# Kernel optimization log

Hardware: AMD Instinct MI355X
Metric: run time of the kernel (lower is better)

## Reference

```python
import jax, jax.numpy as jnp
import numpy as np

N = 100000      # nodes
E = 1600000     # edges (avg degree 16)
IN_DIM = 128
HID = 128
OUT = 10
EPS = 1e-5      # BatchNorm eps


def _lin(key, fan_in, fan_out):
    return jax.random.normal(key, (fan_in, fan_out), jnp.float32) * (1.0 / np.sqrt(fan_in))


def setup_inputs() -> dict:
    key = jax.random.key(0)
    ks = jax.random.split(key, 8)
    x = jax.random.normal(ks[0], (N, IN_DIM), jnp.float32)
    edge_index = jax.random.randint(ks[1], (2, E), 0, N, dtype=jnp.int64)
    return {
        "x": x,
        "edge_index": edge_index,
        "W0": _lin(ks[2], IN_DIM, HID), "b0": jnp.zeros((HID,), jnp.float32),
        "g0": jnp.ones((HID,), jnp.float32), "be0": jnp.zeros((HID,), jnp.float32),
        "W1": _lin(ks[3], HID, HID), "b1": jnp.zeros((HID,), jnp.float32),
        "g1": jnp.ones((HID,), jnp.float32), "be1": jnp.zeros((HID,), jnp.float32),
        "W2": _lin(ks[4], HID, OUT), "b2": jnp.zeros((OUT,), jnp.float32),
    }


def gcn_conv(x, W, b, src, dst, n):
    # PyG GCNConv: add self-loops, symmetric normalization D^-1/2 A D^-1/2.
    # deg includes the self-loop (+1).
    e = src.shape[0]
    deg = jax.ops.segment_sum(jnp.ones((e,), x.dtype), dst, num_segments=n) + 1.0
    dinv = jax.lax.rsqrt(deg)                     # deg >= 1 always
    norm = dinv[src] * dinv[dst]                  # [E]
    h = x @ W                                     # [N, out]
    msgs = h[src] * norm[:, None]                 # gather + scale, [E, out]
    agg = jax.ops.segment_sum(msgs, dst, num_segments=n)
    agg = agg + h * (dinv * dinv)[:, None]        # self-loop contribution
    return agg + b


def batch_norm(x, gamma, beta):
    mu = jnp.mean(x, axis=0)
    var = jnp.mean(jnp.square(x - mu), axis=0)    # biased var, as torch BN training
    return gamma * (x - mu) * jax.lax.rsqrt(var + EPS) + beta


def reference(x, edge_index, W0, b0, g0, be0, W1, b1, g1, be1, W2, b2):
    src, dst = edge_index[0], edge_index[1]
    h = jax.nn.relu(batch_norm(gcn_conv(x, W0, b0, src, dst, N), g0, be0))
    h = jax.nn.relu(batch_norm(gcn_conv(h, W1, b1, src, dst, N), g1, be1))
    return gcn_conv(h, W2, b2, src, dst, N)
```

## Files before the change

kernel.cpp:

```cpp
#include <hip/hip_runtime.h>
#include <hip/hip_bf16.h>

static constexpr int NN  = 100000;
static constexpr int NE  = 1600000;
static constexpr int DIM = 128;
static constexpr int OC  = 10;
static constexpr int BK  = 64;
static constexpr float BN_EPS = 1e-5f;
static constexpr float INVN   = 1.0f / (float)NN;

typedef unsigned short ushortT;
typedef unsigned int uintT;
typedef __attribute__((ext_vector_type(8))) short short8;
typedef __attribute__((ext_vector_type(4))) float floatx4;

__device__ __forceinline__ ushortT f2bf(float f) {
    union { float f; unsigned int i; } c;
    c.f = f;
    unsigned int r = c.i + 0x7FFFu + ((c.i >> 16) & 1u);
    return (ushortT)(r >> 16);
}

__device__ __forceinline__ uintT pack2(float lo, float hi) {
    return (uintT)f2bf(lo) | ((uintT)f2bf(hi) << 16);
}

__device__ __forceinline__ float4 f4fma(const float4 w, const float s, const float4 acc) {
    float4 r;
    r.x = fmaf(w.x, s, acc.x);
    r.y = fmaf(w.y, s, acc.y);
    r.z = fmaf(w.z, s, acc.z);
    r.w = fmaf(w.w, s, acc.w);
    return r;
}

__device__ __forceinline__ void acc8(const uint4 u, float* a) {
    a[0] += __uint_as_float(u.x << 16);
    a[1] += __uint_as_float(u.x & 0xFFFF0000u);
    a[2] += __uint_as_float(u.y << 16);
    a[3] += __uint_as_float(u.y & 0xFFFF0000u);
    a[4] += __uint_as_float(u.z << 16);
    a[5] += __uint_as_float(u.z & 0xFFFF0000u);
    a[6] += __uint_as_float(u.w << 16);
    a[7] += __uint_as_float(u.w & 0xFFFF0000u);
}

__device__ __forceinline__ void fma8(const uint4 u, float s, float* a) {
    a[0] = fmaf(__uint_as_float(u.x << 16),          s, a[0]);
    a[1] = fmaf(__uint_as_float(u.x & 0xFFFF0000u),  s, a[1]);
    a[2] = fmaf(__uint_as_float(u.y << 16),          s, a[2]);
    a[3] = fmaf(__uint_as_float(u.y & 0xFFFF0000u),  s, a[3]);
    a[4] = fmaf(__uint_as_float(u.z << 16),          s, a[4]);
    a[5] = fmaf(__uint_as_float(u.z & 0xFFFF0000u),  s, a[5]);
    a[6] = fmaf(__uint_as_float(u.w << 16),          s, a[6]);
    a[7] = fmaf(__uint_as_float(u.w & 0xFFFF0000u),  s, a[7]);
}

__device__ __forceinline__ void unp8(const uint4 u, float* a) {
    a[0] = __uint_as_float(u.x << 16);
    a[1] = __uint_as_float(u.x & 0xFFFF0000u);
    a[2] = __uint_as_float(u.y << 16);
    a[3] = __uint_as_float(u.y & 0xFFFF0000u);
    a[4] = __uint_as_float(u.z << 16);
    a[5] = __uint_as_float(u.z & 0xFFFF0000u);
    a[6] = __uint_as_float(u.w << 16);
    a[7] = __uint_as_float(u.w & 0xFFFF0000u);
}

__global__ void k_wt(const float* __restrict__ W0, const float* __restrict__ W1,
                     ushortT* __restrict__ WT0, ushortT* __restrict__ WT1,
                     float* __restrict__ stats) {
    int i = blockIdx.x * 256 + threadIdx.x;
    if (i < 512) stats[i] = 0.f;
    int half = i >> 14, r = i & 16383;
    int n = r >> 7, k = r & 127;
    if (half == 0) WT0[r] = f2bf(W0[k * 128 + n]);
    else           WT1[r] = f2bf(W1[k * 128 + n]);
}

__global__ __launch_bounds__(256, 8)
void k_fused(const int* __restrict__ src, const int* __restrict__ dst,
             int* __restrict__ cnt, int* __restrict__ bucket,
             const float* __restrict__ x, const ushortT* __restrict__ WT,
             ushortT* __restrict__ outb)
{
    const int idx = blockIdx.x;
    const int m = idx / 3, r3 = idx - 3 * m;
    if (r3 < 2) {
        int e = (2 * m + r3) * 256 + threadIdx.x;
        if (e < NE) {
            int t = dst[e];
            int slot = atomicAdd(&cnt[t], 1);
            if (slot < BK)
                __hip_atomic_store(&bucket[(size_t)t * BK + slot], src[e],
                                   __ATOMIC_RELAXED, __HIP_MEMORY_SCOPE_AGENT);
        }
        return;
    }
    __shared__ ushortT XS[32 * 136];
    const int tid  = threadIdx.x;
    const int row0 = m * 32;

    #pragma unroll
    for (int i = 0; i < 4; ++i) {
        int id2 = tid + 256 * i;
        int rr = id2 >> 5, c4 = id2 & 31;
        int grow = row0 + rr;
        float4 v = {0.f, 0.f, 0.f, 0.f};
        if (grow < NN) v = ((const float4*)(x + (size_t)grow * DIM))[c4];
        ushort4 o;
        o.x = f2bf(v.x); o.y = f2bf(v.y); o.z = f2bf(v.z); o.w = f2bf(v.w);
        *(ushort4*)(XS + rr * 136 + c4 * 4) = o;
    }
    __syncthreads();

    const int w    = tid >> 6;
    const int lane = tid & 63;
    const int q    = lane >> 4;
    const int mr   = lane & 15;
    const int rw   = (w >> 1) * 16;
    const int ch   = (w & 1) * 64;

    floatx4 acc[4];
    #pragma unroll
    for (int t = 0; t < 4; ++t) { acc[t][0] = 0.f; acc[t][1] = 0.f; acc[t][2] = 0.f; acc[t][3] = 0.f; }

    #pragma unroll
    for (int c = 0; c < 4; ++c) {
        short8 a = *(const short8*)(XS + (rw + mr) * 136 + c * 32 + q * 8);
        #pragma unroll
        for (int t = 0; t < 4; ++t) {
            short8 b = *(const short8*)(WT + (size_t)(ch + t * 16 + mr) * 128 + c * 32 + q * 8);
            acc[t] = __builtin_amdgcn_mfma_f32_16x16x32_bf16(a, b, acc[t], 0, 0, 0);
        }
    }

    #pragma unroll
    for (int rr = 0; rr < 4; ++rr) {
        int grow = row0 + rw + q * 4 + rr;
        if (grow < NN) {
            #pragma unroll
            for (int t = 0; t < 4; ++t)
                outb[(size_t)grow * DIM + ch + t * 16 + mr] = f2bf(acc[t][rr]);
        }
    }
}

__global__ void k_dinv(const int* __restrict__ cnt, float* __restrict__ dinv, int n) {
    int i = blockIdx.x * 256 + threadIdx.x;
    if (i < n) dinv[i] = rsqrtf((float)cnt[i] + 1.0f);
}

template <bool EDGE_SCALE>
__global__ __launch_bounds__(256)
void k_agg_wide(const ushortT* __restrict__ hb, const int* __restrict__ cnt,
                const int* __restrict__ bucket, const float* __restrict__ dinv,
                const float* __restrict__ bias, ushortT* __restrict__ outBb,
                float* __restrict__ stats)
{
    const int lane = threadIdx.x & 63;
    const int w    = threadIdx.x >> 6;
    const int sg   = lane >> 4;
    const int f    = lane & 15;
    const int wid  = blockIdx.x * 4 + w;
    const int nW   = gridDim.x * 4;
    const uint4* h4 = (const uint4*)hb;

    float bl[8];
    #pragma unroll
    for (int i = 0; i < 8; ++i) bl[i] = bias[f * 8 + i];

    float ssum[8], ssq[8];
    #pragma unroll
    for (int i = 0; i < 8; ++i) { ssum[i] = 0.f; ssq[i] = 0.f; }

    for (int n = wid; n < NN; n += nW) {
        int d = cnt[n];
        if (d > BK) d = BK;
        const int* bp = bucket + (size_t)n * BK;
        float a[8];
        #pragma unroll
        for (int i = 0; i < 8; ++i) a[i] = 0.f;

        int j = 0;
        for (; j + 16 <= d; j += 16) {
            int4 pv = *(const int4*)(bp + j + 4 * sg);
            uint4 u0 = h4[(size_t)pv.x * 16 + f];
            uint4 u1 = h4[(size_t)pv.y * 16 + f];
            uint4 u2 = h4[(size_t)pv.z * 16 + f];
            uint4 u3 = h4[(size_t)pv.w * 16 + f];
            if (EDGE_SCALE) {
                float d0 = dinv[pv.x], d1 = dinv[pv.y];
                float d2 = dinv[pv.z], d3 = dinv[pv.w];
                fma8(u0, d0, a);
                fma8(u1, d1, a);
                fma8(u2, d2, a);
                fma8(u3, d3, a);
            } else {
                acc8(u0, a);
                acc8(u1, a);
                acc8(u2, a);
                acc8(u3, a);
            }
        }
        for (; j + 8 <= d; j += 8) {
            int s0 = bp[j + sg];
            int s1 = bp[j + 4 + sg];
            uint4 u0 = h4[(size_t)s0 * 16 + f];
            uint4 u1 = h4[(size_t)s1 * 16 + f];
            if (EDGE_SCALE) {
                float d0 = dinv[s0], d1 = dinv[s1];
                fma8(u0, d0, a);
                fma8(u1, d1, a);
            } else {
                acc8(u0, a);
                acc8(u1, a);
            }
        }
        for (; j < d; j += 4) {
            int e = j + sg;
            if (e < d) {
                int s0 = bp[e];
                uint4 u = h4[(size_t)s0 * 16 + f];
                if (EDGE_SCALE) fma8(u, dinv[s0], a);
                else            acc8(u, a);
            }
        }
        #pragma unroll
        for (int i = 0; i < 8; ++i) {
            a[i] += __shfl_xor(a[i], 16);
            a[i] += __shfl_xor(a[i], 32);
        }
        if (lane < 16) {
            uint4 us = h4[(size_t)n * 16 + f];
            float di = dinv[n];
            if (EDGE_SCALE) fma8(us, di, a);
            else            acc8(us, a);
            float v[8];
            #pragma unroll
            for (int i = 0; i < 8; ++i) v[i] = fmaf(di, a[i], bl[i]);
            uint4 o;
            o.x = pack2(v[0], v[1]);
            o.y = pack2(v[2], v[3]);
            o.z = pack2(v[4], v[5]);
            o.w = pack2(v[6], v[7]);
            ((uint4*)(outBb + (size_t)n * DIM))[f] = o;
            #pragma unroll
            for (int i = 0; i < 8; ++i) {
                ssum[i] += v[i];
                ssq[i]  = fmaf(v[i], v[i], ssq[i]);
            }
        }
    }

    __shared__ float ls[4 * 128], lq[4 * 128];
    if (lane < 16) {
        #pragma unroll
        for (int i = 0; i < 8; ++i) {
            ls[w * 128 + f * 8 + i] = ssum[i];
            lq[w * 128 + f * 8 + i] = ssq[i];
        }
    }
    __syncthreads();
    int t = threadIdx.x;
    if (t < 128) {
        float a = ls[t] + ls[128 + t] + ls[256 + t] + ls[384 + t];
        float b = lq[t] + lq[128 + t] + lq[256 + t] + lq[384 + t];
        unsafeAtomicAdd(&stats[t], a);
        unsafeAtomicAdd(&stats[128 + t], b);
    }
}

__global__ __launch_bounds__(256)
void k_mm128_l1(const ushortT* __restrict__ inb, const ushortT* __restrict__ WT,
                const float* __restrict__ stats, const float* __restrict__ g,
                const float* __restrict__ be, const float* __restrict__ dinv,
                ushortT* __restrict__ outb)
{
    __shared__ ushortT XS[64 * 136];
    __shared__ float CA[128], CD[128];
    const int tid  = threadIdx.x;
    const int row0 = blockIdx.x * 64;

    if (tid < 128) {
        float mu  = stats[tid] * INVN;
        float var = stats[128 + tid] * INVN - mu * mu;
        float a = g[tid] * rsqrtf(var + BN_EPS);
        CA[tid] = a;
        CD[tid] = be[tid] - mu * a;
    }
    __syncthreads();

    #pragma unroll
    for (int i = 0; i < 4; ++i) {
        int idx = tid + 256 * i;
        int r = idx >> 4, c8 = idx & 15;
        int grow = row0 + r;
        uint4 u = {0, 0, 0, 0};
        if (grow < NN) u = ((const uint4*)(inb + (size_t)grow * DIM))[c8];
        float v[8];
        unp8(u, v);
        #pragma unroll
        for (int k = 0; k < 8; ++k)
            v[k] = fmaxf(0.f, fmaf(v[k], CA[c8 * 8 + k], CD[c8 * 8 + k]));
        uint4 o;
        o.x = pack2(v[0], v[1]);
        o.y = pack2(v[2], v[3]);
        o.z = pack2(v[4], v[5]);
        o.w = pack2(v[6], v[7]);
        *(uint4*)(XS + r * 136 + c8 * 8) = o;
    }
    __syncthreads();

    const int w    = tid >> 6;
    const int lane = tid & 63;
    const int q    = lane >> 4;
    const int mr   = lane & 15;
    const int rw   = w * 16;

    floatx4 acc[8];
    #pragma unroll
    for (int t = 0; t < 8; ++t) { acc[t][0] = 0.f; acc[t][1] = 0.f; acc[t][2] = 0.f; acc[t][3] = 0.f; }

    #pragma unroll
    for (int c = 0; c < 4; ++c) {
        short8 a = *(const short8*)(XS + (rw + mr) * 136 + c * 32 + q * 8);
        #pragma unroll
        for (int t = 0; t < 8; ++t) {
            short8 b = *(const short8*)(WT + (size_t)(t * 16 + mr) * 128 + c * 32 + q * 8);
            acc[t] = __builtin_amdgcn_mfma_f32_16x16x32_bf16(a, b, acc[t], 0, 0, 0);
        }
    }

    #pragma unroll
    for (int r = 0; r < 4; ++r) {
        int grow = row0 + rw + q * 4 + r;
        if (grow < NN) {
            float di = dinv[grow];
            #pragma unroll
            for (int t = 0; t < 8; ++t) {
                outb[(size_t)grow * DIM + t * 16 + mr] = f2bf(acc[t][r] * di);
            }
        }
    }
}

__global__ __launch_bounds__(128)
void k_mm_l2(const ushortT* __restrict__ inb, const float* __restrict__ W2,
             const float* __restrict__ stats, const float* __restrict__ g,
             const float* __restrict__ be, const float* __restrict__ dinv,
             ushortT* __restrict__ Cb)
{
    __shared__ float WL[128 * 16];
    __shared__ float XS[32 * 128];
    __shared__ float CA[128], CD[128];
    const int tid  = threadIdx.x;
    const int row0 = blockIdx.x * 32;

    {
        float mu  = stats[tid] * INVN;
        float var = stats[128 + tid] * INVN - mu * mu;
        float a = g[tid] * rsqrtf(var + BN_EPS);
        CA[tid] = a;
        CD[tid] = be[tid] - mu * a;
    }
    for (int idx = tid; idx < 128 * 16; idx += 128) {
        int k = idx >> 4, c = idx & 15;
        WL[idx] = (c < OC) ? W2[k * OC + c] : 0.0f;
    }
    __syncthreads();

    #pragma unroll
    for (int i = 0; i < 4; ++i) {
        int idx = tid + 128 * i;
        int r = idx >> 4, c8 = idx & 15;
        uint4 u = ((const uint4*)(inb + (size_t)(row0 + r) * DIM))[c8];
        float v[8];
        unp8(u, v);
        float* xp = XS + r * 128 + c8 * 8;
        #pragma unroll
        for (int k = 0; k < 8; ++k)
            xp[k] = fmaxf(0.f, fmaf(v[k], CA[c8 * 8 + k], CD[c8 * 8 + k]));
    }
    __syncthreads();

    const int cg = tid & 3;
    const int rg = tid >> 2;
    float4 acc = {0, 0, 0, 0};
    const float4* XS4 = (const float4*)XS;
    const float4* WL4 = (const float4*)WL;
    for (int k = 0; k < 128; k += 4) {
        float4 w0 = WL4[(k + 0) * 4 + cg];
        float4 w1 = WL4[(k + 1) * 4 + cg];
        float4 w2 = WL4[(k + 2) * 4 + cg];
        float4 w3 = WL4[(k + 3) * 4 + cg];
        float4 x = XS4[rg * 32 + (k >> 2)];
        acc = f4fma(w0, x.x, f4fma(w1, x.y, f4fma(w2, x.z, f4fma(w3, x.w, acc))));
    }
    float di = dinv[row0 + rg];
    uint2 o;
    o.x = pack2(acc.x * di, acc.y * di);
    o.y = pack2(acc.z * di, acc.w * di);
    ((uint2*)(Cb + ((size_t)row0 + rg) * 16))[cg] = o;
}

__global__ __launch_bounds__(256)
void k_agg10(const ushortT* __restrict__ Cb, const int* __restrict__ cnt,
             const int* __restrict__ bucket, const float* __restrict__ dinv,
             const float* __restrict__ b2, float* __restrict__ out)
{
    const int lane = threadIdx.x & 63;
    const int sg   = lane >> 3;
    const int f    = lane & 7;
    const int wid  = (blockIdx.x * 256 + threadIdx.x) >> 6;
    const int nW   = gridDim.x * 4;
    const uintT* Cu = (const uintT*)Cb;

    for (int n = wid; n < NN; n += nW) {
        int d = cnt[n];
        if (d > BK) d = BK;
        const int* bp = bucket + (size_t)n * BK;
        float a0 = 0.f, a1 = 0.f;
        for (int j = sg; j < d; j += 8) {
            uintT u = Cu[(size_t)bp[j] * 8 + f];
            a0 += __uint_as_float(u << 16);
            a1 += __uint_as_float(u & 0xFFFF0000u);
        }
        a0 += __shfl_xor(a0, 8);  a1 += __shfl_xor(a1, 8);
        a0 += __shfl_xor(a0, 16); a1 += __shfl_xor(a1, 16);
        a0 += __shfl_xor(a0, 32); a1 += __shfl_xor(a1, 32);
        if (lane < 8) {
            uintT us = Cu[(size_t)n * 8 + f];
            a0 += __uint_as_float(us << 16);
            a1 += __uint_as_float(us & 0xFFFF0000u);
            float di = dinv[n];
            if (2 * f < OC) {
                float2 o;
                o.x = fmaf(di, a0, b2[2 * f]);
                o.y = fmaf(di, a1, b2[2 * f + 1]);
                *(float2*)(out + (size_t)n * OC + 2 * f) = o;
            }
        }
    }
}

extern "C" void kernel_launch(void* const* d_in, const int* in_sizes, int n_in,
                              void* d_out, int out_size, void* d_ws, size_t ws_size,
                              hipStream_t stream) {
    const float* x    = (const float*)d_in[0];
    const int*   ei   = (const int*)d_in[1];
    const int*   srcv = ei;
    const int*   dstv = ei + NE;
    const float* W0  = (const float*)d_in[2];
    const float* b0  = (const float*)d_in[3];
    const float* g0  = (const float*)d_in[4];
    const float* be0 = (const float*)d_in[5];
    const float* W1  = (const float*)d_in[6];
    const float* b1  = (const float*)d_in[7];
    const float* g1  = (const float*)d_in[8];
    const float* be1 = (const float*)d_in[9];
    const float* W2  = (const float*)d_in[10];
    const float* b2  = (const float*)d_in[11];
    float* out = (float*)d_out;

    float* base   = (float*)d_ws;
    int*   cnt    = (int*)base;
    float* dinv   = base + NN;
    float* stats  = base + 2 * NN;
    ushortT* WT0  = (ushortT*)(base + 2 * NN + 512);
    ushortT* WT1  = (ushortT*)(base + 2 * NN + 8704);
    int*   bucket = (int*)(base + 2 * NN + 16896);
    ushortT* A_bf = (ushortT*)(base + 2 * NN + 16896 + (size_t)NN * BK);
    ushortT* B_bf = A_bf + (size_t)NN * DIM;
    ushortT* Cb   = A_bf;

    (void)hipMemsetAsync(cnt, 0, NN * sizeof(int), stream);

    k_wt<<<128, 256, 0, stream>>>(W0, W1, WT0, WT1, stats);

    k_fused<<<9375, 256, 0, stream>>>(srcv, dstv, cnt, bucket, x, WT0, A_bf);
    k_dinv<<<(NN + 255) / 256, 256, 0, stream>>>(cnt, dinv, NN);

    k_agg_wide<true><<<2048, 256, 0, stream>>>(A_bf, cnt, bucket, dinv, b0, B_bf, stats);

    k_mm128_l1<<<(NN + 63) / 64, 256, 0, stream>>>(B_bf, WT1, stats, g0, be0, dinv, A_bf);
    k_agg_wide<false><<<2048, 256, 0, stream>>>(A_bf, cnt, bucket, dinv, b1, B_bf, stats + 256);

    k_mm_l2<<<NN / 32, 128, 0, stream>>>(B_bf, W2, stats + 256, g1, be1, dinv, Cb);
    k_agg10<<<1024, 256, 0, stream>>>(Cb, cnt, bucket, dinv, b2, out);
}
```

Measured before the change: 535.4 us.

## Replace global-atomic edge bucketing with two-pass binned counting sort

Global atomics on per-node counters and scattered bucket stores are replaced by a two-pass scheme. In the first pass, blocks sort 4096-edge chunks into 256-node bins in shared memory and write padded runs to per-bin global regions. In the second pass, one block per bin builds the node buckets with shared-memory atomics and computes degree and dinv, which removes the memset and the separate dinv kernel. The trade-offs are extra passes over edge data and a fixed per-bin capacity that could overflow and silently drop edges on skewed graphs.

```diff
diff --git a/kernel.cpp b/kernel.cpp
--- a/kernel.cpp
+++ b/kernel.cpp
@@ -8,6 +8,10 @@
 static constexpr int BK  = 64;
 static constexpr float BN_EPS = 1e-5f;
 static constexpr float INVN   = 1.0f / (float)NN;
+
+static constexpr int BINS = 391;
+static constexpr int CAP  = 8176;
+static constexpr int P1B  = (NE + 4095) / 4096;
 
 typedef unsigned short ushortT;
 typedef unsigned int uintT;
@@ -71,34 +75,111 @@
                      ushortT* __restrict__ WT0, ushortT* __restrict__ WT1,
                      float* __restrict__ stats) {
     int i = blockIdx.x * 256 + threadIdx.x;
-    if (i < 512) stats[i] = 0.f;
+    if (i < 1024) stats[i] = 0.f;
     int half = i >> 14, r = i & 16383;
     int n = r >> 7, k = r & 127;
     if (half == 0) WT0[r] = f2bf(W0[k * 128 + n]);
     else           WT1[r] = f2bf(W1[k * 128 + n]);
 }
 
-__global__ __launch_bounds__(256, 8)
-void k_fused(const int* __restrict__ src, const int* __restrict__ dst,
-             int* __restrict__ cnt, int* __restrict__ bucket,
-             const float* __restrict__ x, const ushortT* __restrict__ WT,
-             ushortT* __restrict__ outb)
+struct P1S {
+    uint2 stage[4096];
+    int lcnt[BINS];
+    int lbase[512];
+    int lcur[BINS];
+    int goff[BINS];
+};
+union SMu {
+    P1S p1;
+    ushortT xs[32 * 136];
+};
+
+__global__ __launch_bounds__(256)
+void k_p1(const int* __restrict__ src, const int* __restrict__ dst,
+          uint2* __restrict__ gbin, int* __restrict__ gcur,
+          const float* __restrict__ x, const ushortT* __restrict__ WT,
+          ushortT* __restrict__ outb)
 {
+    __shared__ SMu sm;
     const int idx = blockIdx.x;
-    const int m = idx / 3, r3 = idx - 3 * m;
-    if (r3 < 2) {
-        int e = (2 * m + r3) * 256 + threadIdx.x;
-        if (e < NE) {
-            int t = dst[e];
-            int slot = atomicAdd(&cnt[t], 1);
-            if (slot < BK)
-                __hip_atomic_store(&bucket[(size_t)t * BK + slot], src[e],
-                                   __ATOMIC_RELAXED, __HIP_MEMORY_SCOPE_AGENT);
+    const int tid = threadIdx.x;
+    const int d9 = idx / 9;
+    if (idx - 9 * d9 == 0) {
+        P1S& S = sm.p1;
+        const int e00 = d9 * 4096;
+        for (int b = tid; b < BINS; b += 256) S.lcnt[b] = 0;
+        __syncthreads();
+        int4 dv[4], sv[4];
+        bool val[4];
+        #pragma unroll
+        for (int i = 0; i < 4; ++i) {
+            int e0 = e00 + i * 1024 + tid * 4;
+            val[i] = (e0 < NE);
+            if (val[i]) {
+                dv[i] = *(const int4*)(dst + e0);
+                sv[i] = *(const int4*)(src + e0);
+                atomicAdd(&S.lcnt[dv[i].x >> 8], 1);
+                atomicAdd(&S.lcnt[dv[i].y >> 8], 1);
+                atomicAdd(&S.lcnt[dv[i].z >> 8], 1);
+                atomicAdd(&S.lcnt[dv[i].w >> 8], 1);
+            }
+        }
+        __syncthreads();
+        for (int b = tid; b < 512; b += 256) S.lbase[b] = (b < BINS) ? S.lcnt[b] : 0;
+        __syncthreads();
+        for (int off = 1; off < 512; off <<= 1) {
+            int v0 = (tid >= off) ? S.lbase[tid - off] : 0;
+            int c0 = S.lbase[tid];
+            int v1 = S.lbase[tid + 256 - off];
+            int c1 = S.lbase[tid + 256];
+            __syncthreads();
+            S.lbase[tid] = c0 + v0;
+            S.lbase[tid + 256] = c1 + v1;
+            __syncthreads();
+        }
+        for (int b = tid; b < BINS; b += 256) S.lcur[b] = b ? S.lbase[b - 1] : 0;
+        __syncthreads();
+        #pragma unroll
+        for (int i = 0; i < 4; ++i) {
+            if (val[i]) {
+                int p;
+                p = atomicAdd(&S.lcur[dv[i].x >> 8], 1);
+                S.stage[p] = make_uint2((uintT)dv[i].x, (uintT)sv[i].x);
+                p = atomicAdd(&S.lcur[dv[i].y >> 8], 1);
+                S.stage[p] = make_uint2((uintT)dv[i].y, (uintT)sv[i].y);
+                p = atomicAdd(&S.lcur[dv[i].z >> 8], 1);
+                S.stage[p] = make_uint2((uintT)dv[i].z, (uintT)sv[i].z);
+                p = atomicAdd(&S.lcur[dv[i].w >> 8], 1);
+                S.stage[p] = make_uint2((uintT)dv[i].w, (uintT)sv[i].w);
+            }
+        }
+        __syncthreads();
+        for (int b = tid; b < BINS; b += 256) {
+            int c = S.lcnt[b];
+            int r = (c + 7) & ~7;
+            S.goff[b] = r ? atomicAdd(&gcur[b], r) : 0;
+        }
+        __syncthreads();
+        const int total = S.lbase[BINS - 1];
+        for (int p = tid; p < total; p += 256) {
+            uint2 e = S.stage[p];
+            int bin = (int)(e.x >> 8);
+            int eb = bin ? S.lbase[bin - 1] : 0;
+            int gpos = S.goff[bin] + (p - eb);
+            if (gpos < CAP) gbin[(size_t)bin * CAP + gpos] = e;
+        }
+        for (int b = tid; b < BINS; b += 256) {
+            int c = S.lcnt[b];
+            int r = (c + 7) & ~7;
+            for (int q = c; q < r; ++q) {
+                int gpos = S.goff[b] + q;
+                if (gpos < CAP) gbin[(size_t)b * CAP + gpos] = make_uint2(0xFFFFFFFFu, 0u);
+            }
         }
         return;
     }
-    __shared__ ushortT XS[32 * 136];
-    const int tid  = threadIdx.x;
+    const int m = idx - d9 - 1;
+    ushortT* XS = sm.xs;
     const int row0 = m * 32;
 
     #pragma unroll
@@ -146,9 +227,35 @@
     }
 }
 
-__global__ void k_dinv(const int* __restrict__ cnt, float* __restrict__ dinv, int n) {
-    int i = blockIdx.x * 256 + threadIdx.x;
-    if (i < n) dinv[i] = rsqrtf((float)cnt[i] + 1.0f);
+__global__ __launch_bounds__(512)
+void k_p2(const uint2* __restrict__ gbin, const int* __restrict__ gcur,
+          int* __restrict__ bucket, int* __restrict__ cnt,
+          float* __restrict__ dinv)
+{
+    __shared__ int lc[256];
+    const int b = blockIdx.x;
+    const int tid = threadIdx.x;
+    if (tid < 256) lc[tid] = 0;
+    __syncthreads();
+    int cb = gcur[b];
+    if (cb > CAP) cb = CAP;
+    const uint2* gb = gbin + (size_t)b * CAP;
+    for (int p = tid; p < cb; p += 512) {
+        uint2 e = gb[p];
+        if (e.x != 0xFFFFFFFFu) {
+            int slot = atomicAdd(&lc[e.x & 255], 1);
+            if (slot < BK) bucket[(size_t)e.x * BK + slot] = (int)e.y;
+        }
+    }
+    __syncthreads();
+    if (tid < 256) {
+        int n = b * 256 + tid;
+        if (n < NN) {
+            int d = lc[tid];
+            cnt[n] = d;
+            dinv[n] = rsqrtf((float)d + 1.0f);
+        }
+    }
 }
 
 template <bool EDGE_SCALE>
@@ -467,19 +574,19 @@
     int*   cnt    = (int*)base;
     float* dinv   = base + NN;
     float* stats  = base + 2 * NN;
-    ushortT* WT0  = (ushortT*)(base + 2 * NN + 512);
-    ushortT* WT1  = (ushortT*)(base + 2 * NN + 8704);
-    int*   bucket = (int*)(base + 2 * NN + 16896);
-    ushortT* A_bf = (ushortT*)(base + 2 * NN + 16896 + (size_t)NN * BK);
+    int*   gcur   = (int*)(stats + 512);
+    ushortT* WT0  = (ushortT*)(base + 2 * NN + 1024);
+    ushortT* WT1  = (ushortT*)(base + 2 * NN + 9216);
+    int*   bucket = (int*)(base + 2 * NN + 17408);
+    ushortT* A_bf = (ushortT*)(base + 2 * NN + 17408 + (size_t)NN * BK);
     ushortT* B_bf = A_bf + (size_t)NN * DIM;
     ushortT* Cb   = A_bf;
-
-    (void)hipMemsetAsync(cnt, 0, NN * sizeof(int), stream);
+    uint2* gbin   = (uint2*)B_bf;
 
     k_wt<<<128, 256, 0, stream>>>(W0, W1, WT0, WT1, stats);
 
-    k_fused<<<9375, 256, 0, stream>>>(srcv, dstv, cnt, bucket, x, WT0, A_bf);
-    k_dinv<<<(NN + 255) / 256, 256, 0, stream>>>(cnt, dinv, NN);
+    k_p1<<<P1B + 3125, 256, 0, stream>>>(srcv, dstv, gbin, gcur, x, WT0, A_bf);
+    k_p2<<<BINS, 512, 0, stream>>>(gbin, gcur, bucket, cnt, dinv);
 
     k_agg_wide<true><<<2048, 256, 0, stream>>>(A_bf, cnt, bucket, dinv, b0, B_bf, stats);
 
```

Result: faster. 489.3 us (-8.6%).
